# Optimization experiments

Hardware: AMD Instinct MI355X
Metric: run time of the kernel (lower is better)

Reference implementation:

```python
import jax, jax.numpy as jnp
import numpy as np

N_NODES = 100000
N_EDGES = 600000
D = 128          # encoder_output_dim
H = 64           # mlp_edge_model_dim


def setup_inputs() -> dict:
    key = jax.random.key(0)
    k1, k2, k3, k4, k5, k6 = jax.random.split(key, 6)
    node_emb = jax.random.normal(k1, (N_NODES, D), dtype=jnp.float32)
    edge_index = jax.random.randint(k2, (2, N_EDGES), 0, N_NODES, dtype=jnp.int64)
    # MLP params (Linear(2D -> H), Linear(H -> 1)); scale ~ PyTorch default init
    s1 = 1.0 / np.sqrt(2 * D)
    s2 = 1.0 / np.sqrt(H)
    W1 = jax.random.uniform(k3, (2 * D, H), dtype=jnp.float32, minval=-s1, maxval=s1)
    b1 = jax.random.uniform(k4, (H,), dtype=jnp.float32, minval=-s1, maxval=s1)
    W2 = jax.random.uniform(k5, (H, 1), dtype=jnp.float32, minval=-s2, maxval=s2)
    b2 = jax.random.uniform(k6, (1,), dtype=jnp.float32, minval=-s2, maxval=s2)
    return {"node_emb": node_emb, "edge_index": edge_index,
            "W1": W1, "b1": b1, "W2": W2, "b2": b2}


def reference(node_emb, edge_index, W1, b1, W2, b2):
    src, dst = edge_index[0], edge_index[1]
    emb_src = node_emb[src]                      # [E, D] gather
    emb_dst = node_emb[dst]                      # [E, D] gather
    edge_emb = jnp.concatenate([emb_src, emb_dst], axis=1)  # [E, 2D]
    h = jax.nn.relu(edge_emb @ W1 + b1)          # [E, H]
    edge_logits = h @ W2 + b2                    # [E, 1]
    return edge_logits
```

## Files before the change

kernel.cpp:

```cpp
#include <hip/hip_runtime.h>
#include <hip/hip_fp16.h>

#define N_NODES 100000
#define N_EDGES 600000
#define DIM 128
#define HID 64
#define NCHUNK 1563

typedef __attribute__((ext_vector_type(8))) _Float16 half8;
typedef __attribute__((ext_vector_type(4))) _Float16 half4v;
typedef __attribute__((ext_vector_type(4))) float floatx4;
typedef __attribute__((ext_vector_type(4))) unsigned int uint4v;

__device__ __forceinline__ void gload_lds16(const void* g, void* l) {
    __builtin_amdgcn_global_load_lds(
        (const __attribute__((address_space(1))) void*)g,
        (__attribute__((address_space(3))) void*)l, 16, 0, 0);
}

__global__ __launch_bounds__(256) void prep_W(
    const float* __restrict__ W1, __half* __restrict__ W1T)
{
    const int o = (int)(blockIdx.x * blockDim.x + threadIdx.x) * 2;
    if (o >= 128 * 128) return;
    const int c = o >> 7, k = o & 127;
    float w0, w1;
    if (c < HID) { w0 = W1[k * HID + c];               w1 = W1[(k + 1) * HID + c]; }
    else         { w0 = W1[(DIM + k) * HID + c - HID]; w1 = W1[(DIM + k + 1) * HID + c - HID]; }
    W1T[o]     = __float2half(w0);
    W1T[o + 1] = __float2half(w1);
}

__global__ __launch_bounds__(256, 2) void precompute_P(
    const float* __restrict__ node_emb,
    const __half* __restrict__ W1T,
    const float* __restrict__ b1,
    __half* __restrict__ P)
{
    __shared__ float Abuf[2][64 * 128];

    const int tid  = threadIdx.x;
    const int w    = tid >> 6;
    const int lane = tid & 63;
    const int lr   = lane & 15;
    const int q    = lane >> 4;

    half8 wf[8][4];
#pragma unroll
    for (int nt = 0; nt < 8; nt++)
#pragma unroll
        for (int ks = 0; ks < 4; ks++)
            wf[nt][ks] = *(const half8*)(W1T + (size_t)(nt * 16 + lr) * 128 + ks * 32 + q * 8);

#pragma unroll
    for (int nt = 0; nt < 8; nt++)
#pragma unroll
        for (int ks = 0; ks < 4; ks++) {
            uint4v t = __builtin_bit_cast(uint4v, wf[nt][ks]);
            asm volatile("" : "+v"(t));
            wf[nt][ks] = __builtin_bit_cast(half8, t);
        }

    float bias_[4][4];
#pragma unroll
    for (int nt = 0; nt < 4; nt++) {
        const float4 b4 = *(const float4*)(b1 + nt * 16 + q * 4);
        bias_[nt][0] = b4.x; bias_[nt][1] = b4.y;
        bias_[nt][2] = b4.z; bias_[nt][3] = b4.w;
    }

    const int r8   = tid >> 5;
    const int in16 = (tid & 31) << 4;
    const char* nb = (const char*)node_emb;

    for (int rep = 0; rep < 2; rep++) {
        int c = (int)blockIdx.x;
#pragma unroll
        for (int r = 0; r < 8; r++) {
            int row_in = r * 8 + r8;
            int grow = c * 64 + row_in;
            if (grow >= N_NODES) grow = N_NODES - 1;
            const size_t src = (size_t)grow * 512 + (size_t)(in16 ^ ((row_in & 7) << 4));
            gload_lds16(nb + src, (char*)&Abuf[0][0] + (r * 4096 + tid * 16));
        }

        int cur = 0;
        for (; c < NCHUNK; c += (int)gridDim.x, cur ^= 1) {
            const int cnext = c + (int)gridDim.x;
            if (cnext < NCHUNK) {
#pragma unroll
                for (int r = 0; r < 8; r++) {
                    int row_in = r * 8 + r8;
                    int grow = cnext * 64 + row_in;
                    if (grow >= N_NODES) grow = N_NODES - 1;
                    const size_t src = (size_t)grow * 512 + (size_t)(in16 ^ ((row_in & 7) << 4));
                    gload_lds16(nb + src, (char*)&Abuf[cur ^ 1][0] + (r * 4096 + tid * 16));
                }
                asm volatile("s_waitcnt vmcnt(8)" ::: "memory");
            } else {
                asm volatile("s_waitcnt vmcnt(0)" ::: "memory");
            }
            __builtin_amdgcn_s_barrier();

            floatx4 acc[8];
#pragma unroll
            for (int nt = 0; nt < 8; nt++) acc[nt] = (floatx4){0.f, 0.f, 0.f, 0.f};

            const char* Ab = (const char*)&Abuf[cur][0];
            const int rb = w * 16 + lr;
            const int sw = (rb & 7) << 4;
#pragma unroll
            for (int ks = 0; ks < 4; ks++) {
                const int cb = ks * 128 + q * 32;
                const float4 x0 = *(const float4*)(Ab + rb * 512 + ((cb)      ^ sw));
                const float4 x1 = *(const float4*)(Ab + rb * 512 + ((cb + 16) ^ sw));
                half8 af;
                af[0] = (_Float16)x0.x; af[1] = (_Float16)x0.y;
                af[2] = (_Float16)x0.z; af[3] = (_Float16)x0.w;
                af[4] = (_Float16)x1.x; af[5] = (_Float16)x1.y;
                af[6] = (_Float16)x1.z; af[7] = (_Float16)x1.w;
#pragma unroll
                for (int nt = 0; nt < 8; nt++)
                    acc[nt] = __builtin_amdgcn_mfma_f32_16x16x32_f16(wf[nt][ks], af, acc[nt], 0, 0, 0);
            }

            const int grow = c * 64 + w * 16 + lr;
            if (grow < N_NODES) {
                char* prow = (char*)P + (size_t)grow * 256;
#pragma unroll
                for (int m = 0; m < 4; m++) {
                    half8 hh;
#pragma unroll
                    for (int i = 0; i < 4; i++) {
                        float va = acc[2 * m][i];
                        float vb = acc[2 * m + 1][i];
                        if (m < 2) { va += bias_[2 * m][i]; vb += bias_[2 * m + 1][i]; }
                        hh[i]     = (_Float16)va;
                        hh[i + 4] = (_Float16)vb;
                    }
                    *(half8*)(prow + m * 64 + q * 16) = hh;
                }
            }
            __builtin_amdgcn_s_barrier();
        }
    }
}

__device__ inline bool detect_int64(const int* e32) {
    int orv = 0;
#pragma unroll
    for (int k = 0; k < 8; k++) orv |= e32[2 * k + 1];
    return orv == 0;
}

__global__ __launch_bounds__(256) void edge_mlp(
    const __half* __restrict__ P,
    const void* __restrict__ eidx_raw,
    const float* __restrict__ W2,
    const float* __restrict__ b2,
    float* __restrict__ out)
{
    const int* e32 = (const int*)eidx_raw;
    const long long* e64 = (const long long*)eidx_raw;
    const bool is64 = detect_int64(e32);

    const int tid  = threadIdx.x;
    const int lane = tid & 63;
    const int j    = lane & 15;
    const int grp  = lane >> 4;
    const int hbase = ((j >> 3) << 5) + ((j & 1) << 4) + (((j >> 1) & 3) << 2);
    const float4 w2 = *(const float4*)(W2 + hbase);
    const float b2v = b2[0];

    const int gwid   = (int)((blockIdx.x * blockDim.x + tid) >> 6);
    const int nwaves = (int)((gridDim.x * blockDim.x) >> 6);

    const half4v zero = {(_Float16)0, (_Float16)0, (_Float16)0, (_Float16)0};

    for (int base = gwid * 16; base < N_EDGES; base += nwaves * 16) {
        int s[4], d[4];
#pragma unroll
        for (int u = 0; u < 4; u++) {
            const int e = base + 4 * u + grp;
            if (is64) { s[u] = (int)e64[e]; d[u] = (int)e64[N_EDGES + e]; }
            else      { s[u] = e32[e];      d[u] = e32[N_EDGES + e]; }
        }
        half4v av[4], bv[4];
#pragma unroll
        for (int u = 0; u < 4; u++) {
            av[u] = *(const half4v*)(P + (size_t)s[u] * 128 + 4 * j);
            bv[u] = *(const half4v*)(P + (size_t)d[u] * 128 + 64 + 4 * j);
        }
#pragma unroll
        for (int u = 0; u < 4; u++) {
            const half4v t = av[u] + bv[u];
            const half4v r = __builtin_elementwise_max(t, zero);
            float acc = (float)r[0] * w2.x + (float)r[1] * w2.y
                      + (float)r[2] * w2.z + (float)r[3] * w2.w;
#pragma unroll
            for (int off = 8; off >= 1; off >>= 1)
                acc += __shfl_xor(acc, off, 64);
            if (j == 0) out[base + 4 * u + grp] = acc + b2v;
        }
    }
}

__global__ __launch_bounds__(256) void edge_mlp_direct(
    const float* __restrict__ node_emb,
    const void* __restrict__ eidx_raw,
    const float* __restrict__ W1,
    const float* __restrict__ b1,
    const float* __restrict__ W2,
    const float* __restrict__ b2,
    float* __restrict__ out)
{
    const int* e32 = (const int*)eidx_raw;
    const long long* e64 = (const long long*)eidx_raw;
    const bool is64 = detect_int64(e32);

    const int lane = threadIdx.x & 63;
    const float w2  = W2[lane];
    const float b2v = b2[0];
    const int gwid   = (int)((blockIdx.x * blockDim.x + threadIdx.x) >> 6);
    const int nwaves = (int)((gridDim.x * blockDim.x) >> 6);

    for (int e = gwid; e < N_EDGES; e += nwaves) {
        int s, d;
        if (is64) { s = (int)e64[e]; d = (int)e64[N_EDGES + e]; }
        else      { s = e32[e];      d = e32[N_EDGES + e]; }
        const float* es = node_emb + (size_t)s * DIM;
        const float* ed = node_emb + (size_t)d * DIM;
        float acc = b1[lane];
        for (int k = 0; k < DIM; k++) {
            acc += es[k] * W1[k * HID + lane];
            acc += ed[k] * W1[(DIM + k) * HID + lane];
        }
        float t = fmaxf(acc, 0.f) * w2;
#pragma unroll
        for (int off = 32; off >= 1; off >>= 1)
            t += __shfl_xor(t, off, 64);
        if (lane == 0) out[e] = t + b2v;
    }
}

extern "C" void kernel_launch(void* const* d_in, const int* in_sizes, int n_in,
                              void* d_out, int out_size, void* d_ws, size_t ws_size,
                              hipStream_t stream) {
    const float* node_emb = (const float*)d_in[0];
    const void*  eidx     = d_in[1];
    const float* W1       = (const float*)d_in[2];
    const float* b1       = (const float*)d_in[3];
    const float* W2       = (const float*)d_in[4];
    const float* b2       = (const float*)d_in[5];
    float* out = (float*)d_out;

    const size_t wt_off = 32u * 1024 * 1024;
    const size_t need   = wt_off + 128 * 128 * sizeof(__half);

    if (ws_size >= need) {
        __half* P   = (__half*)d_ws;
        __half* W1T = (__half*)((char*)d_ws + wt_off);
        prep_W<<<32, 256, 0, stream>>>(W1, W1T);
        precompute_P<<<512, 256, 0, stream>>>(node_emb, W1T, b1, P);
        edge_mlp<<<2048, 256, 0, stream>>>(P, eidx, W2, b2, out);
    } else {
        edge_mlp_direct<<<4096, 256, 0, stream>>>(node_emb, eidx, W1, b1, W2, b2, out);
    }
}
```

Baseline: 63.43 us.

## Restructure node projection to one chunk per block and widen edge batching

The node projection kernel now launches one block per 64-node chunk instead of a persistent grid with double-buffered LDS. It loads the weights in two 64-column halves to cut register pressure, and raises launch bounds to allow more resident blocks. It also drops an outer loop that recomputed the whole projection twice. The edge kernel now handles 8 edges per lane group per iteration instead of 4, so more gathers are in flight at once. The trade-offs are losing the cross-chunk prefetch overlap, re-reading the weight fragments for each half, and higher register use in the edge kernel.

```diff
diff --git a/kernel.cpp b/kernel.cpp
--- a/kernel.cpp
+++ b/kernel.cpp
@@ -31,118 +31,104 @@
     W1T[o + 1] = __float2half(w1);
 }
 
-__global__ __launch_bounds__(256, 2) void precompute_P(
+__global__ __launch_bounds__(256, 5) void precompute_P(
     const float* __restrict__ node_emb,
     const __half* __restrict__ W1T,
     const float* __restrict__ b1,
     __half* __restrict__ P)
 {
-    __shared__ float Abuf[2][64 * 128];
+    __shared__ char Abuf[64 * 512];
 
     const int tid  = threadIdx.x;
     const int w    = tid >> 6;
     const int lane = tid & 63;
     const int lr   = lane & 15;
     const int q    = lane >> 4;
-
-    half8 wf[8][4];
-#pragma unroll
-    for (int nt = 0; nt < 8; nt++)
-#pragma unroll
-        for (int ks = 0; ks < 4; ks++)
-            wf[nt][ks] = *(const half8*)(W1T + (size_t)(nt * 16 + lr) * 128 + ks * 32 + q * 8);
-
-#pragma unroll
-    for (int nt = 0; nt < 8; nt++)
-#pragma unroll
-        for (int ks = 0; ks < 4; ks++) {
-            uint4v t = __builtin_bit_cast(uint4v, wf[nt][ks]);
-            asm volatile("" : "+v"(t));
-            wf[nt][ks] = __builtin_bit_cast(half8, t);
-        }
-
-    float bias_[4][4];
-#pragma unroll
-    for (int nt = 0; nt < 4; nt++) {
-        const float4 b4 = *(const float4*)(b1 + nt * 16 + q * 4);
-        bias_[nt][0] = b4.x; bias_[nt][1] = b4.y;
-        bias_[nt][2] = b4.z; bias_[nt][3] = b4.w;
-    }
-
+    const int c    = (int)blockIdx.x;
+
+    const char* nb = (const char*)node_emb;
     const int r8   = tid >> 5;
     const int in16 = (tid & 31) << 4;
-    const char* nb = (const char*)node_emb;
-
-    for (int rep = 0; rep < 2; rep++) {
-        int c = (int)blockIdx.x;
-#pragma unroll
-        for (int r = 0; r < 8; r++) {
-            int row_in = r * 8 + r8;
-            int grow = c * 64 + row_in;
-            if (grow >= N_NODES) grow = N_NODES - 1;
-            const size_t src = (size_t)grow * 512 + (size_t)(in16 ^ ((row_in & 7) << 4));
-            gload_lds16(nb + src, (char*)&Abuf[0][0] + (r * 4096 + tid * 16));
-        }
-
-        int cur = 0;
-        for (; c < NCHUNK; c += (int)gridDim.x, cur ^= 1) {
-            const int cnext = c + (int)gridDim.x;
-            if (cnext < NCHUNK) {
-#pragma unroll
-                for (int r = 0; r < 8; r++) {
-                    int row_in = r * 8 + r8;
-                    int grow = cnext * 64 + row_in;
-                    if (grow >= N_NODES) grow = N_NODES - 1;
-                    const size_t src = (size_t)grow * 512 + (size_t)(in16 ^ ((row_in & 7) << 4));
-                    gload_lds16(nb + src, (char*)&Abuf[cur ^ 1][0] + (r * 4096 + tid * 16));
+
+#pragma unroll
+    for (int r = 0; r < 8; r++) {
+        int row_in = r * 8 + r8;
+        int grow = c * 64 + row_in;
+        if (grow >= N_NODES) grow = N_NODES - 1;
+        const size_t src = (size_t)grow * 512 + (size_t)(in16 ^ ((row_in & 7) << 4));
+        gload_lds16(nb + src, &Abuf[r * 4096 + tid * 16]);
+    }
+
+    const int rb   = w * 16 + lr;
+    const int sw   = (lr & 7) << 4;
+    const int grow = c * 64 + rb;
+    char* prow = (char*)P + (size_t)grow * 256;
+    const bool wr = (grow < N_NODES);
+
+#pragma unroll 1
+    for (int h = 0; h < 2; h++) {
+        half8 wf[4][4];
+#pragma unroll
+        for (int nt = 0; nt < 4; nt++)
+#pragma unroll
+            for (int ks = 0; ks < 4; ks++)
+                wf[nt][ks] = *(const half8*)(W1T + (size_t)(h * 64 + nt * 16 + lr) * 128 + ks * 32 + q * 8);
+#pragma unroll
+        for (int nt = 0; nt < 4; nt++)
+#pragma unroll
+            for (int ks = 0; ks < 4; ks++) {
+                uint4v t = __builtin_bit_cast(uint4v, wf[nt][ks]);
+                asm volatile("" : "+v"(t));
+                wf[nt][ks] = __builtin_bit_cast(half8, t);
+            }
+
+        if (h == 0) {
+            asm volatile("s_waitcnt vmcnt(0)" ::: "memory");
+            __builtin_amdgcn_s_barrier();
+        }
+
+        floatx4 acc[4];
+#pragma unroll
+        for (int nt = 0; nt < 4; nt++) acc[nt] = (floatx4){0.f, 0.f, 0.f, 0.f};
+
+#pragma unroll
+        for (int ks = 0; ks < 4; ks++) {
+            const int cb = ks * 128 + q * 32;
+            const float4 x0 = *(const float4*)(Abuf + rb * 512 + ((cb)      ^ sw));
+            const float4 x1 = *(const float4*)(Abuf + rb * 512 + ((cb + 16) ^ sw));
+            half8 af;
+            af[0] = (_Float16)x0.x; af[1] = (_Float16)x0.y;
+            af[2] = (_Float16)x0.z; af[3] = (_Float16)x0.w;
+            af[4] = (_Float16)x1.x; af[5] = (_Float16)x1.y;
+            af[6] = (_Float16)x1.z; af[7] = (_Float16)x1.w;
+#pragma unroll
+            for (int nt = 0; nt < 4; nt++)
+                acc[nt] = __builtin_amdgcn_mfma_f32_16x16x32_f16(wf[nt][ks], af, acc[nt], 0, 0, 0);
+        }
+
+        if (wr) {
+#pragma unroll
+            for (int mm = 0; mm < 2; mm++) {
+                float va0 = acc[2 * mm][0], va1 = acc[2 * mm][1],
+                      va2 = acc[2 * mm][2], va3 = acc[2 * mm][3];
+                float vb0 = acc[2 * mm + 1][0], vb1 = acc[2 * mm + 1][1],
+                      vb2 = acc[2 * mm + 1][2], vb3 = acc[2 * mm + 1][3];
+                if (h == 0) {
+                    const float4 ba = *(const float4*)(b1 + (2 * mm) * 16 + q * 4);
+                    const float4 bb = *(const float4*)(b1 + (2 * mm + 1) * 16 + q * 4);
+                    va0 += ba.x; va1 += ba.y; va2 += ba.z; va3 += ba.w;
+                    vb0 += bb.x; vb1 += bb.y; vb2 += bb.z; vb3 += bb.w;
                 }
-                asm volatile("s_waitcnt vmcnt(8)" ::: "memory");
-            } else {
-                asm volatile("s_waitcnt vmcnt(0)" ::: "memory");
+                half8 hh;
+                hh[0] = (_Float16)va0; hh[1] = (_Float16)va1;
+                hh[2] = (_Float16)va2; hh[3] = (_Float16)va3;
+                hh[4] = (_Float16)vb0; hh[5] = (_Float16)vb1;
+                hh[6] = (_Float16)vb2; hh[7] = (_Float16)vb3;
+                const int m = 2 * h + mm;
+                *(half8*)(prow + m * 64 + q * 16) = hh;
             }
-            __builtin_amdgcn_s_barrier();
-
-            floatx4 acc[8];
-#pragma unroll
-            for (int nt = 0; nt < 8; nt++) acc[nt] = (floatx4){0.f, 0.f, 0.f, 0.f};
-
-            const char* Ab = (const char*)&Abuf[cur][0];
-            const int rb = w * 16 + lr;
-            const int sw = (rb & 7) << 4;
-#pragma unroll
-            for (int ks = 0; ks < 4; ks++) {
-                const int cb = ks * 128 + q * 32;
-                const float4 x0 = *(const float4*)(Ab + rb * 512 + ((cb)      ^ sw));
-                const float4 x1 = *(const float4*)(Ab + rb * 512 + ((cb + 16) ^ sw));
-                half8 af;
-                af[0] = (_Float16)x0.x; af[1] = (_Float16)x0.y;
-                af[2] = (_Float16)x0.z; af[3] = (_Float16)x0.w;
-                af[4] = (_Float16)x1.x; af[5] = (_Float16)x1.y;
-                af[6] = (_Float16)x1.z; af[7] = (_Float16)x1.w;
-#pragma unroll
-                for (int nt = 0; nt < 8; nt++)
-                    acc[nt] = __builtin_amdgcn_mfma_f32_16x16x32_f16(wf[nt][ks], af, acc[nt], 0, 0, 0);
-            }
-
-            const int grow = c * 64 + w * 16 + lr;
-            if (grow < N_NODES) {
-                char* prow = (char*)P + (size_t)grow * 256;
-#pragma unroll
-                for (int m = 0; m < 4; m++) {
-                    half8 hh;
-#pragma unroll
-                    for (int i = 0; i < 4; i++) {
-                        float va = acc[2 * m][i];
-                        float vb = acc[2 * m + 1][i];
-                        if (m < 2) { va += bias_[2 * m][i]; vb += bias_[2 * m + 1][i]; }
-                        hh[i]     = (_Float16)va;
-                        hh[i + 4] = (_Float16)vb;
-                    }
-                    *(half8*)(prow + m * 64 + q * 16) = hh;
-                }
-            }
-            __builtin_amdgcn_s_barrier();
-        }
+        }
+        __builtin_amdgcn_sched_barrier(0);
     }
 }
 
@@ -177,22 +163,22 @@
 
     const half4v zero = {(_Float16)0, (_Float16)0, (_Float16)0, (_Float16)0};
 
-    for (int base = gwid * 16; base < N_EDGES; base += nwaves * 16) {
-        int s[4], d[4];
-#pragma unroll
-        for (int u = 0; u < 4; u++) {
+    for (int base = gwid * 32; base < N_EDGES; base += nwaves * 32) {
+        int s[8], d[8];
+#pragma unroll
+        for (int u = 0; u < 8; u++) {
             const int e = base + 4 * u + grp;
             if (is64) { s[u] = (int)e64[e]; d[u] = (int)e64[N_EDGES + e]; }
             else      { s[u] = e32[e];      d[u] = e32[N_EDGES + e]; }
         }
-        half4v av[4], bv[4];
-#pragma unroll
-        for (int u = 0; u < 4; u++) {
+        half4v av[8], bv[8];
+#pragma unroll
+        for (int u = 0; u < 8; u++) {
             av[u] = *(const half4v*)(P + (size_t)s[u] * 128 + 4 * j);
             bv[u] = *(const half4v*)(P + (size_t)d[u] * 128 + 64 + 4 * j);
         }
 #pragma unroll
-        for (int u = 0; u < 4; u++) {
+        for (int u = 0; u < 8; u++) {
             const half4v t = av[u] + bv[u];
             const half4v r = __builtin_elementwise_max(t, zero);
             float acc = (float)r[0] * w2.x + (float)r[1] * w2.y
@@ -261,7 +247,7 @@
         __half* P   = (__half*)d_ws;
         __half* W1T = (__half*)((char*)d_ws + wt_off);
         prep_W<<<32, 256, 0, stream>>>(W1, W1T);
-        precompute_P<<<512, 256, 0, stream>>>(node_emb, W1T, b1, P);
+        precompute_P<<<NCHUNK, 256, 0, stream>>>(node_emb, W1T, b1, P);
         edge_mlp<<<2048, 256, 0, stream>>>(P, eidx, W2, b2, out);
     } else {
         edge_mlp_direct<<<4096, 256, 0, stream>>>(node_emb, eidx, W1, b1, W2, b2, out);
```

New measurement: 65.42 us. 3.1% more time.
